# Kernel optimization log

Measured on AMD Instinct MI355X. Metric: run time of the kernel, lower is better.

The kernel has to match this reference:

```python
import jax, jax.numpy as jnp
import numpy as np
from jax import lax

D_MODEL = 1024
D_INNER = 2 * D_MODEL          # expand = 2
D_STATE = 16
D_CONV = 4
DT_RANK = D_MODEL // 16        # ceil(1024/16) = 64
LN_EPS = 1e-6


def setup_inputs() -> dict:
    key = jax.random.key(0)
    ks = jax.random.split(key, 12)
    s = 0.02
    x = jax.random.normal(ks[0], (2, 2048, D_MODEL), dtype=jnp.float32)
    ln_w = jnp.ones((D_MODEL,), jnp.float32)
    ln_b = jnp.zeros((D_MODEL,), jnp.float32)
    in_proj_w = jax.random.normal(ks[1], (2 * D_INNER, D_MODEL), jnp.float32) * s
    conv_w = jax.random.normal(ks[2], (D_INNER, 1, D_CONV), jnp.float32) * s   # depthwise
    conv_b = jax.random.normal(ks[3], (D_INNER,), jnp.float32) * s
    x_proj_w = jax.random.normal(ks[4], (DT_RANK + 2 * D_STATE, D_INNER), jnp.float32) * s
    dt_proj_w = jax.random.normal(ks[5], (D_INNER, DT_RANK), jnp.float32) * s
    dt_proj_b = jax.random.normal(ks[6], (D_INNER,), jnp.float32) * s
    # A_log init: log(arange(1, d_state+1)) broadcast over channels (mamba default)
    A_log = jnp.log(jnp.broadcast_to(jnp.arange(1, D_STATE + 1, dtype=jnp.float32),
                                     (D_INNER, D_STATE)))
    D_param = jnp.ones((D_INNER,), jnp.float32)
    out_proj_w = jax.random.normal(ks[7], (D_MODEL, D_INNER), jnp.float32) * s
    return {"x": x, "ln_w": ln_w, "ln_b": ln_b, "in_proj_w": in_proj_w,
            "conv_w": conv_w, "conv_b": conv_b, "x_proj_w": x_proj_w,
            "dt_proj_w": dt_proj_w, "dt_proj_b": dt_proj_b, "A_log": A_log,
            "D_param": D_param, "out_proj_w": out_proj_w}


def _layer_norm(x, w, b):
    mu = jnp.mean(x, axis=-1, keepdims=True)
    var = jnp.mean(jnp.square(x - mu), axis=-1, keepdims=True)
    return (x - mu) * lax.rsqrt(var + LN_EPS) * w + b


def _mamba_block(x, ln_w, ln_b, in_proj_w, conv_w, conv_b, x_proj_w,
                 dt_proj_w, dt_proj_b, A_log, D_param, out_proj_w):
    Bsz, L, _ = x.shape
    h = _layer_norm(x, ln_w, ln_b)
    xz = jnp.einsum('bld,ed->ble', h, in_proj_w)            # (B, L, 2*d_inner)
    xi, z = jnp.split(xz, 2, axis=-1)
    # causal depthwise conv1d (pad left d_conv-1, truncate to L) + silu
    xc = lax.conv_general_dilated(
        xi.transpose(0, 2, 1), conv_w, window_strides=(1,),
        padding=[(D_CONV - 1, 0)], feature_group_count=D_INNER)  # (B, d_inner, L)
    u = jax.nn.silu(xc + conv_b[None, :, None]).transpose(0, 2, 1)  # (B, L, d_inner)
    # input-dependent dt, B, C
    x_dbl = jnp.einsum('bld,ed->ble', u, x_proj_w)
    dt = x_dbl[..., :DT_RANK]
    Bm = x_dbl[..., DT_RANK:DT_RANK + D_STATE]               # (B, L, N)
    Cm = x_dbl[..., DT_RANK + D_STATE:]                      # (B, L, N)
    delta = jax.nn.softplus(jnp.einsum('blr,dr->bld', dt, dt_proj_w) + dt_proj_b)
    A = -jnp.exp(A_log)                                      # (d_inner, N)
    deltaA = jnp.exp(jnp.einsum('bld,dn->bldn', delta, A))   # (B, L, d_inner, N)
    deltaBu = jnp.einsum('bld,bln,bld->bldn', delta, Bm, u)  # (B, L, d_inner, N)

    def step(hprev, inp):
        dA, dBu, c = inp                                     # (B,d,n),(B,d,n),(B,n)
        hnew = dA * hprev + dBu
        y = jnp.einsum('bdn,bn->bd', hnew, c)
        return hnew, y

    h0 = jnp.zeros((Bsz, D_INNER, D_STATE), x.dtype)
    _, ys = lax.scan(step, h0, (deltaA.transpose(1, 0, 2, 3),
                                deltaBu.transpose(1, 0, 2, 3),
                                Cm.transpose(1, 0, 2)))
    y = ys.transpose(1, 0, 2)                                # (B, L, d_inner)
    y = y + u * D_param
    y = y * jax.nn.silu(z)
    out = jnp.einsum('ble,de->bld', y, out_proj_w)
    return out + x                                           # residual (dropout p=0)


def reference(x, ln_w, ln_b, in_proj_w, conv_w, conv_b, x_proj_w,
              dt_proj_w, dt_proj_b, A_log, D_param, out_proj_w):
    return _mamba_block(x, ln_w, ln_b, in_proj_w, conv_w, conv_b, x_proj_w,
                        dt_proj_w, dt_proj_b, A_log, D_param, out_proj_w)
```

## Files before the change

kernel.cpp:

```cpp
#include <hip/hip_runtime.h>
#include <math.h>

#define BSZ 2
#define LSEQ 2048
#define DM 1024
#define DI 2048
#define DS 16
#define RK 64
#define ROWS (BSZ*LSEQ)
#define NC 32
#define CL 64

typedef __attribute__((ext_vector_type(8))) short bf16x8;
typedef __attribute__((ext_vector_type(4))) float f32x4;

static __device__ __forceinline__ unsigned short f2bf(float f) {
  unsigned u = __builtin_bit_cast(unsigned, f);
  unsigned r = (u + 0x7fffu + ((u >> 16) & 1u)) >> 16;
  return (unsigned short)r;
}
static __device__ __forceinline__ float bf2f(unsigned short s) {
  return __builtin_bit_cast(float, (unsigned)s << 16);
}

static __device__ __forceinline__ void gload_lds16(const unsigned short* g, unsigned short* l) {
  __builtin_amdgcn_global_load_lds(
      (const __attribute__((address_space(1))) unsigned int*)g,
      (__attribute__((address_space(3))) unsigned int*)l, 16, 0, 0);
}

__global__ __launch_bounds__(256) void ln_kernel(const float* __restrict__ x,
    const float* __restrict__ w, const float* __restrict__ b,
    unsigned short* __restrict__ h) {
  int row = blockIdx.x;
  int tid = threadIdx.x;
  const float* xr = x + (size_t)row * DM;
  float4 v = *(const float4*)(xr + tid * 4);
  float s  = v.x + v.y + v.z + v.w;
  float s2 = v.x*v.x + v.y*v.y + v.z*v.z + v.w*v.w;
  #pragma unroll
  for (int m = 32; m >= 1; m >>= 1) {
    s  += __shfl_xor(s, m);
    s2 += __shfl_xor(s2, m);
  }
  __shared__ float ss[4], ss2[4];
  int wid = tid >> 6;
  if ((tid & 63) == 0) { ss[wid] = s; ss2[wid] = s2; }
  __syncthreads();
  s  = ss[0] + ss[1] + ss[2] + ss[3];
  s2 = ss2[0] + ss2[1] + ss2[2] + ss2[3];
  float mu  = s * (1.0f / DM);
  float var = s2 * (1.0f / DM) - mu * mu;
  float inv = rsqrtf(var + 1e-6f);
  float4 wv = *(const float4*)(w + tid * 4);
  float4 bv = *(const float4*)(b + tid * 4);
  ushort4 o;
  o.x = f2bf((v.x - mu) * inv * wv.x + bv.x);
  o.y = f2bf((v.y - mu) * inv * wv.y + bv.y);
  o.z = f2bf((v.z - mu) * inv * wv.z + bv.z);
  o.w = f2bf((v.w - mu) * inv * wv.w + bv.w);
  *(ushort4*)(h + (size_t)row * DM + tid * 4) = o;
}

__global__ __launch_bounds__(256) void f2bf_kernel(const float* __restrict__ in,
    unsigned short* __restrict__ out) {
  int i = (blockIdx.x * 256 + threadIdx.x) * 4;
  float4 v = *(const float4*)(in + i);
  ushort4 o;
  o.x = f2bf(v.x); o.y = f2bf(v.y); o.z = f2bf(v.z); o.w = f2bf(v.w);
  *(ushort4*)(out + i) = o;
}

__global__ __launch_bounds__(256) void gemm_mfma(
    const unsigned short* __restrict__ A, int lda,
    const unsigned short* __restrict__ B, int ldb,
    float* __restrict__ C, int ldc,
    const float* __restrict__ Res, int K) {
  __shared__ unsigned short As[128 * 32];
  __shared__ unsigned short Bs[128 * 32];
  const int tid = threadIdx.x;
  const int wid = tid >> 6;
  const int lane = tid & 63;
  const int bm = blockIdx.y * 128;
  const int bn = blockIdx.x * 128;
  const int wm = (wid >> 1) * 64;
  const int wn = (wid & 1) * 64;
  const int frow = lane & 15;
  const int koff = (lane >> 4) * 8;
  const int srow = lane >> 2;
  const int skol = (lane & 3) * 8;

  f32x4 acc[4][4] = {};

  for (int k0 = 0; k0 < K; k0 += 32) {
    if (k0 > 0) __syncthreads();
    #pragma unroll
    for (int i = 0; i < 2; i++) {
      int br = wid * 32 + i * 16;
      gload_lds16(A + (size_t)(bm + br + srow) * lda + k0 + skol, &As[br * 32]);
      gload_lds16(B + (size_t)(bn + br + srow) * ldb + k0 + skol, &Bs[br * 32]);
    }
    __syncthreads();
    bf16x8 af[4], bfr[4];
    #pragma unroll
    for (int m = 0; m < 4; m++)
      af[m] = *(const bf16x8*)&As[(wm + m * 16 + frow) * 32 + koff];
    #pragma unroll
    for (int n = 0; n < 4; n++)
      bfr[n] = *(const bf16x8*)&Bs[(wn + n * 16 + frow) * 32 + koff];
    #pragma unroll
    for (int m = 0; m < 4; m++)
      #pragma unroll
      for (int n = 0; n < 4; n++)
        acc[m][n] = __builtin_amdgcn_mfma_f32_16x16x32_bf16(af[m], bfr[n], acc[m][n], 0, 0, 0);
  }

  const int crow0 = (lane >> 4) * 4;
  const int ccol  = lane & 15;
  #pragma unroll
  for (int m = 0; m < 4; m++) {
    #pragma unroll
    for (int n = 0; n < 4; n++) {
      #pragma unroll
      for (int j = 0; j < 4; j++) {
        size_t off = (size_t)(bm + wm + m * 16 + crow0 + j) * ldc + bn + wn + n * 16 + ccol;
        float r = Res ? Res[off] : 0.0f;
        C[off] = acc[m][n][j] + r;
      }
    }
  }
}

__global__ __launch_bounds__(256) void conv_silu_kernel(
    const float* __restrict__ xz, const float* __restrict__ cw,
    const float* __restrict__ cb, float* __restrict__ u,
    unsigned short* __restrict__ u_bf) {
  size_t idx = (size_t)blockIdx.x * 256 + threadIdx.x;
  int c = (int)(idx & (DI - 1));
  int l = (int)((idx >> 11) & (LSEQ - 1));
  int b = (int)(idx >> 22);
  float acc = cb[c];
  const float* w4 = cw + c * 4;
  #pragma unroll
  for (int k = 0; k < 4; k++) {
    int ls = l + k - 3;
    if (ls >= 0) acc += w4[k] * xz[(size_t)(b * LSEQ + ls) * (2 * DI) + c];
  }
  float sg = 1.0f / (1.0f + __expf(-acc));
  float v = acc * sg;
  u[idx] = v;
  u_bf[idx] = f2bf(v);
}

__global__ __launch_bounds__(256) void xproj_mfma(
    const unsigned short* __restrict__ A,
    const unsigned short* __restrict__ B,
    float* __restrict__ P) {
  __shared__ unsigned short As[128 * 32];
  __shared__ unsigned short Bs[96 * 32];
  const int tid = threadIdx.x;
  const int wid = tid >> 6;
  const int lane = tid & 63;
  const int ks = blockIdx.x;
  const int bm = blockIdx.y * 128;
  const int wm = wid * 32;
  const int frow = lane & 15;
  const int koff = (lane >> 4) * 8;
  const int srow = lane >> 2;
  const int skol = (lane & 3) * 8;

  f32x4 acc[2][6] = {};

  for (int ki = 0; ki < 8; ki++) {
    int k0 = ks * 256 + ki * 32;
    if (ki > 0) __syncthreads();
    #pragma unroll
    for (int i = 0; i < 2; i++) {
      int br = wid * 32 + i * 16;
      gload_lds16(A + (size_t)(bm + br + srow) * DI + k0 + skol, &As[br * 32]);
    }
    if (wid < 3) {
      #pragma unroll
      for (int i = 0; i < 2; i++) {
        int br = wid * 32 + i * 16;
        gload_lds16(B + (size_t)(br + srow) * DI + k0 + skol, &Bs[br * 32]);
      }
    }
    __syncthreads();
    bf16x8 af[2], bfr[6];
    #pragma unroll
    for (int m = 0; m < 2; m++)
      af[m] = *(const bf16x8*)&As[(wm + m * 16 + frow) * 32 + koff];
    #pragma unroll
    for (int n = 0; n < 6; n++)
      bfr[n] = *(const bf16x8*)&Bs[(n * 16 + frow) * 32 + koff];
    #pragma unroll
    for (int m = 0; m < 2; m++)
      #pragma unroll
      for (int n = 0; n < 6; n++)
        acc[m][n] = __builtin_amdgcn_mfma_f32_16x16x32_bf16(af[m], bfr[n], acc[m][n], 0, 0, 0);
  }

  const int crow0 = (lane >> 4) * 4;
  const int ccol  = lane & 15;
  #pragma unroll
  for (int m = 0; m < 2; m++)
    #pragma unroll
    for (int n = 0; n < 6; n++)
      #pragma unroll
      for (int j = 0; j < 4; j++)
        P[((size_t)ks * ROWS + bm + wm + m * 16 + crow0 + j) * 96 + n * 16 + ccol] =
            acc[m][n][j];
}

__global__ __launch_bounds__(256) void xproj_reduce(
    const float* __restrict__ P, float* __restrict__ xdbl) {
  int e = blockIdx.x * 256 + threadIdx.x;
  float s = 0.f;
  #pragma unroll
  for (int ks = 0; ks < 8; ks++)
    s += P[(size_t)ks * (ROWS * 96) + e];
  xdbl[e] = s;
}

__global__ __launch_bounds__(256) void dtproj_gemm(
    const float* __restrict__ xdbl, const float* __restrict__ dtw,
    const float* __restrict__ dtb, float* __restrict__ delta) {
  __shared__ float As[64][64];
  __shared__ float Bs[64][64];
  const int bm = blockIdx.y * 64;
  const int bn = blockIdx.x * 64;
  const int tid = threadIdx.x;
  const int tm = (tid >> 4) << 2;
  const int tn = (tid & 15) << 2;
  const int lr = tid >> 2;
  const int lc = (tid & 3) << 4;
  #pragma unroll
  for (int j = 0; j < 4; j++) {
    float4 v = *(const float4*)(xdbl + (size_t)(bm + lr) * 96 + lc + j * 4);
    As[lc + j*4 + 0][lr] = v.x; As[lc + j*4 + 1][lr] = v.y;
    As[lc + j*4 + 2][lr] = v.z; As[lc + j*4 + 3][lr] = v.w;
    float4 w = *(const float4*)(dtw + (size_t)(bn + lr) * 64 + lc + j * 4);
    Bs[lc + j*4 + 0][lr] = w.x; Bs[lc + j*4 + 1][lr] = w.y;
    Bs[lc + j*4 + 2][lr] = w.z; Bs[lc + j*4 + 3][lr] = w.w;
  }
  __syncthreads();
  float acc[4][4] = {};
  #pragma unroll 16
  for (int k = 0; k < 64; k++) {
    float4 a = *(const float4*)&As[k][tm];
    float4 b = *(const float4*)&Bs[k][tn];
    acc[0][0] += a.x * b.x; acc[0][1] += a.x * b.y;
    acc[0][2] += a.x * b.z; acc[0][3] += a.x * b.w;
    acc[1][0] += a.y * b.x; acc[1][1] += a.y * b.y;
    acc[1][2] += a.y * b.z; acc[1][3] += a.y * b.w;
    acc[2][0] += a.z * b.x; acc[2][1] += a.z * b.y;
    acc[2][2] += a.z * b.z; acc[2][3] += a.z * b.w;
    acc[3][0] += a.w * b.x; acc[3][1] += a.w * b.y;
    acc[3][2] += a.w * b.z; acc[3][3] += a.w * b.w;
  }
  #pragma unroll
  for (int i = 0; i < 4; i++) {
    #pragma unroll
    for (int j = 0; j < 4; j++) {
      float v = acc[i][j] + dtb[bn + tn + j];
      v = (v > 20.0f) ? v : log1pf(__expf(v));
      delta[(size_t)(bm + tm + i) * DI + bn + tn + j] = v;
    }
  }
}


__global__ __launch_bounds__(256) void scan1_kernel(
    const float* __restrict__ delta, const float* __restrict__ u,
    const float* __restrict__ xdbl, const float* __restrict__ Alog,
    const float* __restrict__ Dp, float* __restrict__ xz) {
  const int d = blockIdx.x * 256 + threadIdx.x;
  const int c = blockIdx.y;
  const int b = blockIdx.z;
  __shared__ float sBC[CL][32];
  {
    int tt = threadIdx.x >> 2;
    int jj = (threadIdx.x & 3) * 8;
    const float* xr = xdbl + (size_t)(b * LSEQ + c * CL + tt) * 96 + 64 + jj;
    float4 q0 = *(const float4*)(xr);
    float4 q1 = *(const float4*)(xr + 4);
    sBC[tt][jj + 0] = q0.x; sBC[tt][jj + 1] = q0.y;
    sBC[tt][jj + 2] = q0.z; sBC[tt][jj + 3] = q0.w;
    sBC[tt][jj + 4] = q1.x; sBC[tt][jj + 5] = q1.y;
    sBC[tt][jj + 6] = q1.z; sBC[tt][jj + 7] = q1.w;
  }
  float a[16], h[16], P[16];
  #pragma unroll
  for (int j = 0; j < 4; j++) {
    float4 av = *(const float4*)(Alog + d * 16 + j * 4);
    a[j*4+0] = -__expf(av.x); a[j*4+1] = -__expf(av.y);
    a[j*4+2] = -__expf(av.z); a[j*4+3] = -__expf(av.w);
  }
  #pragma unroll
  for (int n = 0; n < 16; n++) { h[n] = 0.f; P[n] = 1.f; }
  const float dpv = Dp[d];
  unsigned short* yb = (unsigned short*)xz;
  __syncthreads();
  for (int l = 0; l < CL; l++) {
    size_t r = (size_t)(b * LSEQ + c * CL + l);
    float dv = delta[r * DI + d];
    float uv = u[r * DI + d];
    float acc = uv * dpv;
    float dvu = dv * uv;
    #pragma unroll
    for (int n = 0; n < 16; n++) {
      float dA = __expf(dv * a[n]);
      h[n] = dA * h[n] + dvu * sBC[l][n];
      P[n] *= dA;
      acc += h[n] * sBC[l][16 + n];
    }
    yb[r * 8192 + d] = f2bf(acc);
  }
  int base = ((b * NC + c) * DI + d) * 16;
  float* Srow = xz + (size_t)(base >> 9) * 4096 + 1024 + (base & 511);
  #pragma unroll
  for (int n = 0; n < 16; n++) { Srow[n] = h[n]; Srow[512 + n] = P[n]; }
}

__global__ __launch_bounds__(256) void scan2_kernel(float* __restrict__ xz) {
  int gid = blockIdx.x * 256 + threadIdx.x;
  int b = gid >> 15;
  int dn = gid & 32767;
  float h = 0.f;
  for (int c = 0; c < NC; c++) {
    int idx = (b * NC + c) * 32768 + dn;
    float* Srow = xz + (size_t)(idx >> 9) * 4096 + 1024 + (idx & 511);
    float s = Srow[0], p = Srow[512];
    Srow[0] = h;
    h = p * h + s;
  }
}

__global__ __launch_bounds__(256) void scan3_kernel(
    const float* __restrict__ delta, const float* __restrict__ xdbl,
    const float* __restrict__ Alog, float* __restrict__ xz) {
  const int d = blockIdx.x * 256 + threadIdx.x;
  const int c = blockIdx.y;
  const int b = blockIdx.z;
  __shared__ float sC[CL][16];
  if (c > 0) {
    int tt = threadIdx.x >> 1;
    int jj = (threadIdx.x & 1) * 8;
    const float* xr = xdbl + (size_t)(b * LSEQ + c * CL + tt) * 96 + 80 + jj;
    float4 q0 = *(const float4*)(xr);
    float4 q1 = *(const float4*)(xr + 4);
    sC[tt][jj + 0] = q0.x; sC[tt][jj + 1] = q0.y;
    sC[tt][jj + 2] = q0.z; sC[tt][jj + 3] = q0.w;
    sC[tt][jj + 4] = q1.x; sC[tt][jj + 5] = q1.y;
    sC[tt][jj + 6] = q1.z; sC[tt][jj + 7] = q1.w;
  }
  unsigned short* yb = (unsigned short*)xz;
  float a[16], p[16];
  {
    int base = ((b * NC + c) * DI + d) * 16;
    const float* Srow = xz + (size_t)(base >> 9) * 4096 + 1024 + (base & 511);
    #pragma unroll
    for (int j = 0; j < 4; j++) {
      float4 av = *(const float4*)(Alog + d * 16 + j * 4);
      a[j*4+0] = -__expf(av.x); a[j*4+1] = -__expf(av.y);
      a[j*4+2] = -__expf(av.z); a[j*4+3] = -__expf(av.w);
      float4 pv = *(const float4*)(Srow + j * 4);
      p[j*4+0] = pv.x; p[j*4+1] = pv.y; p[j*4+2] = pv.z; p[j*4+3] = pv.w;
    }
  }
  __syncthreads();
  for (int l = 0; l < CL; l++) {
    size_t r = (size_t)(b * LSEQ + c * CL + l);
    float corr = 0.f;
    if (c > 0) {
      float dv = delta[r * DI + d];
      #pragma unroll
      for (int n = 0; n < 16; n++) {
        p[n] *= __expf(dv * a[n]);
        corr += p[n] * sC[l][n];
      }
    }
    float y = bf2f(yb[r * 8192 + d]) + corr;
    float zv = xz[r * 4096 + 2048 + d];
    float g = zv / (1.f + __expf(-zv));
    yb[r * 8192 + d] = f2bf(y * g);
  }
}

extern "C" void kernel_launch(void* const* d_in, const int* in_sizes, int n_in,
                              void* d_out, int out_size, void* d_ws, size_t ws_size,
                              hipStream_t stream) {
  const float* x     = (const float*)d_in[0];
  const float* ln_w  = (const float*)d_in[1];
  const float* ln_b  = (const float*)d_in[2];
  const float* w_in  = (const float*)d_in[3];
  const float* cw    = (const float*)d_in[4];
  const float* cb    = (const float*)d_in[5];
  const float* xpw   = (const float*)d_in[6];
  const float* dtw   = (const float*)d_in[7];
  const float* dtb   = (const float*)d_in[8];
  const float* Alog  = (const float*)d_in[9];
  const float* Dp    = (const float*)d_in[10];
  const float* w_out = (const float*)d_in[11];
  float* out = (float*)d_out;

  unsigned char* wsb = (unsigned char*)d_ws;
  unsigned short* h_bf     = (unsigned short*)wsb;
  unsigned short* w_out_bf = (unsigned short*)wsb;
  float* xz    = (float*)(wsb + (8u << 20));
  float* u     = (float*)(wsb + (72u << 20));
  float* delta = (float*)(wsb + (104u << 20));
  unsigned short* w_in_bf = (unsigned short*)(wsb + (104u << 20));
  float* Pbuf  = (float*)(wsb + (104u << 20));
  unsigned short* u_bf = (unsigned short*)(wsb + (120u << 20));
  float* xdbl  = (float*)(wsb + (136u << 20));
  unsigned short* xpw_bf = (unsigned short*)(wsb + (138u << 20));

  f2bf_kernel<<<4096, 256, 0, stream>>>(w_in, w_in_bf);
  f2bf_kernel<<<192, 256, 0, stream>>>(xpw, xpw_bf);
  ln_kernel<<<ROWS, 256, 0, stream>>>(x, ln_w, ln_b, h_bf);
  gemm_mfma<<<dim3(32, 32), 256, 0, stream>>>(h_bf, DM, w_in_bf, DM, xz, 2 * DI, nullptr, DM);
  f2bf_kernel<<<2048, 256, 0, stream>>>(w_out, w_out_bf);
  conv_silu_kernel<<<(ROWS * DI) / 256, 256, 0, stream>>>(xz, cw, cb, u, u_bf);
  xproj_mfma<<<dim3(8, 32), 256, 0, stream>>>(u_bf, xpw_bf, Pbuf);
  xproj_reduce<<<(ROWS * 96) / 256, 256, 0, stream>>>(Pbuf, xdbl);
  dtproj_gemm<<<dim3(32, 64), 256, 0, stream>>>(xdbl, dtw, dtb, delta);
  scan1_kernel<<<dim3(8, NC, 2), 256, 0, stream>>>(delta, u, xdbl, Alog, Dp, xz);
  scan2_kernel<<<256, 256, 0, stream>>>(xz);
  scan3_kernel<<<dim3(8, NC, 2), 256, 0, stream>>>(delta, xdbl, Alog, xz);
  gemm_mfma<<<dim3(8, 32), 256, 0, stream>>>((const unsigned short*)xz, 2 * 4096, w_out_bf, DI,
                                             out, DM, x, DI);
}
```

Before: 437.3 us.

## Store in_proj output and conv activations in bf16, merge weight casts, swizzle GEMM tiles

The in_proj GEMM now writes xz as bf16 instead of fp32. Conv_silu drops the fp32 u copy and writes only bf16, and scan1 reads bf16 u. The three weight conversions are merged into one launch, the GEMM block order is swizzled for better L2 locality, and the chunk-state buffers move to dedicated contiguous arrays. The goal is to cut global memory traffic on the large intermediates, at the cost of extra rounding of xz, z and u to bf16.

Result: faster. 415.3 us (-5.0%).

```diff
diff --git a/kernel.cpp b/kernel.cpp
--- a/kernel.cpp
+++ b/kernel.cpp
@@ -62,27 +62,38 @@
   *(ushort4*)(h + (size_t)row * DM + tid * 4) = o;
 }
 
-__global__ __launch_bounds__(256) void f2bf_kernel(const float* __restrict__ in,
-    unsigned short* __restrict__ out) {
-  int i = (blockIdx.x * 256 + threadIdx.x) * 4;
-  float4 v = *(const float4*)(in + i);
+__global__ __launch_bounds__(256) void f2bf3_kernel(
+    const float* __restrict__ w_in, unsigned short* __restrict__ w_in_bf,
+    const float* __restrict__ w_out, unsigned short* __restrict__ w_out_bf,
+    const float* __restrict__ xpw, unsigned short* __restrict__ xpw_bf) {
+  int blk = blockIdx.x;
+  const float* src; unsigned short* dst; int base;
+  if (blk < 4096)      { src = w_in;  dst = w_in_bf;  base = blk; }
+  else if (blk < 6144) { src = w_out; dst = w_out_bf; base = blk - 4096; }
+  else                 { src = xpw;   dst = xpw_bf;   base = blk - 6144; }
+  int i = (base * 256 + threadIdx.x) * 4;
+  float4 v = *(const float4*)(src + i);
   ushort4 o;
   o.x = f2bf(v.x); o.y = f2bf(v.y); o.z = f2bf(v.z); o.w = f2bf(v.w);
-  *(ushort4*)(out + i) = o;
-}
-
+  *(ushort4*)(dst + i) = o;
+}
+
+template<bool BF16_OUT>
 __global__ __launch_bounds__(256) void gemm_mfma(
     const unsigned short* __restrict__ A, int lda,
     const unsigned short* __restrict__ B, int ldb,
-    float* __restrict__ C, int ldc,
+    void* __restrict__ Cout, int ldc,
     const float* __restrict__ Res, int K) {
   __shared__ unsigned short As[128 * 32];
   __shared__ unsigned short Bs[128 * 32];
   const int tid = threadIdx.x;
   const int wid = tid >> 6;
   const int lane = tid & 63;
-  const int bm = blockIdx.y * 128;
-  const int bn = blockIdx.x * 128;
+  const int nwg = gridDim.x * gridDim.y;
+  const int flat = blockIdx.y * gridDim.x + blockIdx.x;
+  const int swz = (flat & 7) * (nwg >> 3) + (flat >> 3);
+  const int bm = (swz / gridDim.x) * 128;
+  const int bn = (swz % gridDim.x) * 128;
   const int wm = (wid >> 1) * 64;
   const int wn = (wid & 1) * 64;
   const int frow = lane & 15;
@@ -124,17 +135,20 @@
       #pragma unroll
       for (int j = 0; j < 4; j++) {
         size_t off = (size_t)(bm + wm + m * 16 + crow0 + j) * ldc + bn + wn + n * 16 + ccol;
-        float r = Res ? Res[off] : 0.0f;
-        C[off] = acc[m][n][j] + r;
+        if constexpr (BF16_OUT) {
+          ((unsigned short*)Cout)[off] = f2bf(acc[m][n][j]);
+        } else {
+          float r = Res ? Res[off] : 0.0f;
+          ((float*)Cout)[off] = acc[m][n][j] + r;
+        }
       }
     }
   }
 }
 
 __global__ __launch_bounds__(256) void conv_silu_kernel(
-    const float* __restrict__ xz, const float* __restrict__ cw,
-    const float* __restrict__ cb, float* __restrict__ u,
-    unsigned short* __restrict__ u_bf) {
+    const unsigned short* __restrict__ xz, const float* __restrict__ cw,
+    const float* __restrict__ cb, unsigned short* __restrict__ u_bf) {
   size_t idx = (size_t)blockIdx.x * 256 + threadIdx.x;
   int c = (int)(idx & (DI - 1));
   int l = (int)((idx >> 11) & (LSEQ - 1));
@@ -144,12 +158,10 @@
   #pragma unroll
   for (int k = 0; k < 4; k++) {
     int ls = l + k - 3;
-    if (ls >= 0) acc += w4[k] * xz[(size_t)(b * LSEQ + ls) * (2 * DI) + c];
+    if (ls >= 0) acc += w4[k] * bf2f(xz[(size_t)(b * LSEQ + ls) * 4096 + c]);
   }
   float sg = 1.0f / (1.0f + __expf(-acc));
-  float v = acc * sg;
-  u[idx] = v;
-  u_bf[idx] = f2bf(v);
+  u_bf[idx] = f2bf(acc * sg);
 }
 
 __global__ __launch_bounds__(256) void xproj_mfma(
@@ -272,9 +284,10 @@
 
 
 __global__ __launch_bounds__(256) void scan1_kernel(
-    const float* __restrict__ delta, const float* __restrict__ u,
+    const float* __restrict__ delta, const unsigned short* __restrict__ u_bf,
     const float* __restrict__ xdbl, const float* __restrict__ Alog,
-    const float* __restrict__ Dp, float* __restrict__ xz) {
+    const float* __restrict__ Dp, unsigned short* __restrict__ y,
+    float* __restrict__ Sbuf, float* __restrict__ Pbuf) {
   const int d = blockIdx.x * 256 + threadIdx.x;
   const int c = blockIdx.y;
   const int b = blockIdx.z;
@@ -300,12 +313,11 @@
   #pragma unroll
   for (int n = 0; n < 16; n++) { h[n] = 0.f; P[n] = 1.f; }
   const float dpv = Dp[d];
-  unsigned short* yb = (unsigned short*)xz;
   __syncthreads();
   for (int l = 0; l < CL; l++) {
     size_t r = (size_t)(b * LSEQ + c * CL + l);
     float dv = delta[r * DI + d];
-    float uv = u[r * DI + d];
+    float uv = bf2f(u_bf[r * DI + d]);
     float acc = uv * dpv;
     float dvu = dv * uv;
     #pragma unroll
@@ -315,31 +327,31 @@
       P[n] *= dA;
       acc += h[n] * sBC[l][16 + n];
     }
-    yb[r * 8192 + d] = f2bf(acc);
+    y[r * 4096 + d] = f2bf(acc);
   }
   int base = ((b * NC + c) * DI + d) * 16;
-  float* Srow = xz + (size_t)(base >> 9) * 4096 + 1024 + (base & 511);
-  #pragma unroll
-  for (int n = 0; n < 16; n++) { Srow[n] = h[n]; Srow[512 + n] = P[n]; }
-}
-
-__global__ __launch_bounds__(256) void scan2_kernel(float* __restrict__ xz) {
+  #pragma unroll
+  for (int n = 0; n < 16; n++) { Sbuf[base + n] = h[n]; Pbuf[base + n] = P[n]; }
+}
+
+__global__ __launch_bounds__(256) void scan2_kernel(
+    float* __restrict__ Sbuf, const float* __restrict__ Pbuf) {
   int gid = blockIdx.x * 256 + threadIdx.x;
   int b = gid >> 15;
   int dn = gid & 32767;
   float h = 0.f;
   for (int c = 0; c < NC; c++) {
-    int idx = (b * NC + c) * 32768 + dn;
-    float* Srow = xz + (size_t)(idx >> 9) * 4096 + 1024 + (idx & 511);
-    float s = Srow[0], p = Srow[512];
-    Srow[0] = h;
+    size_t idx = (size_t)(b * NC + c) * 32768 + dn;
+    float s = Sbuf[idx], p = Pbuf[idx];
+    Sbuf[idx] = h;
     h = p * h + s;
   }
 }
 
 __global__ __launch_bounds__(256) void scan3_kernel(
     const float* __restrict__ delta, const float* __restrict__ xdbl,
-    const float* __restrict__ Alog, float* __restrict__ xz) {
+    const float* __restrict__ Alog, const float* __restrict__ Sbuf,
+    unsigned short* __restrict__ xzb) {
   const int d = blockIdx.x * 256 + threadIdx.x;
   const int c = blockIdx.y;
   const int b = blockIdx.z;
@@ -355,17 +367,15 @@
     sC[tt][jj + 4] = q1.x; sC[tt][jj + 5] = q1.y;
     sC[tt][jj + 6] = q1.z; sC[tt][jj + 7] = q1.w;
   }
-  unsigned short* yb = (unsigned short*)xz;
   float a[16], p[16];
   {
     int base = ((b * NC + c) * DI + d) * 16;
-    const float* Srow = xz + (size_t)(base >> 9) * 4096 + 1024 + (base & 511);
     #pragma unroll
     for (int j = 0; j < 4; j++) {
       float4 av = *(const float4*)(Alog + d * 16 + j * 4);
       a[j*4+0] = -__expf(av.x); a[j*4+1] = -__expf(av.y);
       a[j*4+2] = -__expf(av.z); a[j*4+3] = -__expf(av.w);
-      float4 pv = *(const float4*)(Srow + j * 4);
+      float4 pv = *(const float4*)(Sbuf + base + j * 4);
       p[j*4+0] = pv.x; p[j*4+1] = pv.y; p[j*4+2] = pv.z; p[j*4+3] = pv.w;
     }
   }
@@ -381,10 +391,10 @@
         corr += p[n] * sC[l][n];
       }
     }
-    float y = bf2f(yb[r * 8192 + d]) + corr;
-    float zv = xz[r * 4096 + 2048 + d];
+    float yv = bf2f(xzb[r * 4096 + d]) + corr;
+    float zv = bf2f(xzb[r * 4096 + 2048 + d]);
     float g = zv / (1.f + __expf(-zv));
-    yb[r * 8192 + d] = f2bf(y * g);
+    xzb[r * 4096 + d] = f2bf(yv * g);
   }
 }
 
@@ -406,29 +416,27 @@
   float* out = (float*)d_out;
 
   unsigned char* wsb = (unsigned char*)d_ws;
-  unsigned short* h_bf     = (unsigned short*)wsb;
-  unsigned short* w_out_bf = (unsigned short*)wsb;
-  float* xz    = (float*)(wsb + (8u << 20));
-  float* u     = (float*)(wsb + (72u << 20));
-  float* delta = (float*)(wsb + (104u << 20));
-  unsigned short* w_in_bf = (unsigned short*)(wsb + (104u << 20));
-  float* Pbuf  = (float*)(wsb + (104u << 20));
-  unsigned short* u_bf = (unsigned short*)(wsb + (120u << 20));
-  float* xdbl  = (float*)(wsb + (136u << 20));
-  unsigned short* xpw_bf = (unsigned short*)(wsb + (138u << 20));
-
-  f2bf_kernel<<<4096, 256, 0, stream>>>(w_in, w_in_bf);
-  f2bf_kernel<<<192, 256, 0, stream>>>(xpw, xpw_bf);
+  unsigned short* h_bf  = (unsigned short*)wsb;
+  unsigned short* xz    = (unsigned short*)(wsb + (8u   << 20));
+  unsigned short* u_bf  = (unsigned short*)(wsb + (40u  << 20));
+  float* delta          = (float*)(wsb + (56u  << 20));
+  float* PbufX          = (float*)(wsb + (88u  << 20));
+  float* Sbuf           = (float*)(wsb + (104u << 20));
+  float* Pbuf           = (float*)(wsb + (112u << 20));
+  float* xdbl           = (float*)(wsb + (120u << 20));
+  unsigned short* xpw_bf  = (unsigned short*)(wsb + (122u << 20));
+  unsigned short* w_in_bf = (unsigned short*)(wsb + (123u << 20));
+  unsigned short* w_out_bf= (unsigned short*)(wsb + (131u << 20));
+
+  f2bf3_kernel<<<6336, 256, 0, stream>>>(w_in, w_in_bf, w_out, w_out_bf, xpw, xpw_bf);
   ln_kernel<<<ROWS, 256, 0, stream>>>(x, ln_w, ln_b, h_bf);
-  gemm_mfma<<<dim3(32, 32), 256, 0, stream>>>(h_bf, DM, w_in_bf, DM, xz, 2 * DI, nullptr, DM);
-  f2bf_kernel<<<2048, 256, 0, stream>>>(w_out, w_out_bf);
-  conv_silu_kernel<<<(ROWS * DI) / 256, 256, 0, stream>>>(xz, cw, cb, u, u_bf);
-  xproj_mfma<<<dim3(8, 32), 256, 0, stream>>>(u_bf, xpw_bf, Pbuf);
-  xproj_reduce<<<(ROWS * 96) / 256, 256, 0, stream>>>(Pbuf, xdbl);
+  gemm_mfma<true><<<dim3(32, 32), 256, 0, stream>>>(h_bf, DM, w_in_bf, DM, xz, 4096, nullptr, DM);
+  conv_silu_kernel<<<(ROWS * DI) / 256, 256, 0, stream>>>(xz, cw, cb, u_bf);
+  xproj_mfma<<<dim3(8, 32), 256, 0, stream>>>(u_bf, xpw_bf, PbufX);
+  xproj_reduce<<<(ROWS * 96) / 256, 256, 0, stream>>>(PbufX, xdbl);
   dtproj_gemm<<<dim3(32, 64), 256, 0, stream>>>(xdbl, dtw, dtb, delta);
-  scan1_kernel<<<dim3(8, NC, 2), 256, 0, stream>>>(delta, u, xdbl, Alog, Dp, xz);
-  scan2_kernel<<<256, 256, 0, stream>>>(xz);
-  scan3_kernel<<<dim3(8, NC, 2), 256, 0, stream>>>(delta, xdbl, Alog, xz);
-  gemm_mfma<<<dim3(8, 32), 256, 0, stream>>>((const unsigned short*)xz, 2 * 4096, w_out_bf, DI,
-                                             out, DM, x, DI);
-}
+  scan1_kernel<<<dim3(8, NC, 2), 256, 0, stream>>>(delta, u_bf, xdbl, Alog, Dp, xz, Sbuf, Pbuf);
+  scan2_kernel<<<256, 256, 0, stream>>>(Sbuf, Pbuf);
+  scan3_kernel<<<dim3(8, NC, 2), 256, 0, stream>>>(delta, xdbl, Alog, Sbuf, xz);
+  gemm_mfma<false><<<dim3(8, 32), 256, 0, stream>>>(xz, 4096, w_out_bf, DI, out, DM, x, DI);
+}
```
